# Kernel optimization log

Hardware: AMD Instinct MI355X
Metric: run time of the kernel (lower is better)

## Reference

```python
import jax, jax.numpy as jnp
import numpy as np

NUM_HEADS = 16


def setup_inputs() -> dict:
    key = jax.random.key(0)
    ks = jax.random.split(key, 5)
    b, s, d = 2, 2048, 1024
    std = (2.0 / (d + d)) ** 0.5
    x = jax.random.normal(ks[0], (b, s, d), dtype=jnp.float32)
    Wq = jax.random.normal(ks[1], (d, d), dtype=jnp.float32) * std
    Wk = jax.random.normal(ks[2], (d, d), dtype=jnp.float32) * std
    Wv = jax.random.normal(ks[3], (d, d), dtype=jnp.float32) * std
    Wo = jax.random.normal(ks[4], (d, d), dtype=jnp.float32) * std
    return {"x": x, "Wq": Wq, "Wk": Wk, "Wv": Wv, "Wo": Wo}


def reference(x, Wq, Wk, Wv, Wo):
    b, s, d = x.shape
    h = NUM_HEADS
    dk = d // h
    # projections: bias-free x @ W (W is [in, out])
    def split_heads(t):
        return t.reshape(b, s, h, dk).transpose(0, 2, 1, 3)  # b h s dk
    q = split_heads(x @ Wq)
    k = split_heads(x @ Wk)
    v = split_heads(x @ Wv)
    scale = 1.0 / jnp.sqrt(jnp.asarray(dk, dtype=x.dtype))
    scores = jnp.einsum('bhqd,bhkd->bhqk', q, k) * scale  # b h s s
    causal = jnp.tril(jnp.ones((s, s), dtype=bool))
    scores = jnp.where(causal, scores, -jnp.inf)
    probs = jax.nn.softmax(scores, axis=-1)
    out = jnp.einsum('bhqk,bhkd->bhqd', probs, v)
    out = out.transpose(0, 2, 1, 3).reshape(b, s, d)  # b s (h dk)
    return out @ Wo
```

## Files before the change

### kernel.cpp

```cpp
#include <hip/hip_runtime.h>

typedef unsigned short u16;
typedef unsigned int   u32;

using bf16x8 = __attribute__((ext_vector_type(8))) __bf16;
using bf16x4 = __attribute__((ext_vector_type(4))) __bf16;
using f32x4  = __attribute__((ext_vector_type(4))) float;
using s16x4  = __attribute__((ext_vector_type(4))) short;

#define NH    16
#define DKH   64
#define SEQ   2048
#define BAT   2
#define DMOD  1024

#define QSCALE 0.18033688011112042f

__device__ __forceinline__ u16 f2bf(float f) {
  union { float f; u32 u; } v; v.f = f;
  u32 r = v.u + 0x7fffu + ((v.u >> 16) & 1u);
  return (u16)(r >> 16);
}

__device__ __forceinline__ u32 pack2bf(float a, float b) {
  union { float f; u32 u; } x, y; x.f = a; y.f = b;
  u32 ua = x.u + 0x7fffu + ((x.u >> 16) & 1u);
  u32 ub = y.u + 0x7fffu + ((y.u >> 16) & 1u);
  return __builtin_amdgcn_perm(ub, ua, 0x07060302u);
}

__device__ __forceinline__ s16x4 pk4bf(float a, float b, float c, float d) {
  union { bf16x4 bv; s16x4 sv; } u;
  u.bv[0] = (__bf16)a; u.bv[1] = (__bf16)b; u.bv[2] = (__bf16)c; u.bv[3] = (__bf16)d;
  return u.sv;
}

#if __has_builtin(__builtin_amdgcn_exp2f)
#define EXP2(x) __builtin_amdgcn_exp2f(x)
#else
#define EXP2(x) exp2f(x)
#endif

#if __has_builtin(__builtin_amdgcn_mfma_f32_16x16x16bf16_1k)
__device__ __forceinline__ f32x4 mfma16(s16x4 a, s16x4 b, f32x4 c) {
  return __builtin_amdgcn_mfma_f32_16x16x16bf16_1k(a, b, c, 0, 0, 0);
}
#else
__device__ __forceinline__ f32x4 mfma16(s16x4 a, s16x4 b, f32x4 c) {
  f32x4 d;
  asm volatile("v_mfma_f32_16x16x16_bf16 %0, %1, %2, %3\n\ts_nop 7\n\ts_nop 7"
               : "=v"(d) : "v"(a), "v"(b), "v"(c));
  return d;
}
#endif

typedef const __attribute__((address_space(1))) u32 glb_u32;
typedef __attribute__((address_space(3))) u32 lds_u32;
__device__ __forceinline__ void gload16(const u16* g, u16* l) {
  __builtin_amdgcn_global_load_lds((glb_u32*)(const void*)g, (lds_u32*)(void*)l, 16, 0, 0);
}

__global__ __launch_bounds__(256) void transpose_all(const float* __restrict__ Wq,
                                                     const float* __restrict__ Wk,
                                                     const float* __restrict__ Wv,
                                                     const float* __restrict__ Wo,
                                                     u16* __restrict__ Wt) {
  __shared__ u16 t[32][33];
  const float* W = blockIdx.z == 0 ? Wq : blockIdx.z == 1 ? Wk : blockIdx.z == 2 ? Wv : Wo;
  u16* o = Wt + (size_t)blockIdx.z * DMOD * DMOD;
  int bx = blockIdx.x * 32, by = blockIdx.y * 32;
  int x = threadIdx.x, y = threadIdx.y;
  #pragma unroll
  for (int i = 0; i < 32; i += 8)
    t[y + i][x] = f2bf(W[(size_t)(by + y + i) * DMOD + bx + x]);
  __syncthreads();
  #pragma unroll
  for (int i = 0; i < 32; i += 8)
    o[(size_t)(bx + y + i) * DMOD + by + x] = t[x][y + i];
}

__global__ __launch_bounds__(256) void convert_x(const float* __restrict__ x,
                                                 u16* __restrict__ xb) {
  size_t i = ((size_t)blockIdx.x * 256 + threadIdx.x) * 8;
  float4 f0 = *(const float4*)(x + i);
  float4 f1 = *(const float4*)(x + i + 4);
  uint4 o;
  o.x = pack2bf(f0.x, f0.y); o.y = pack2bf(f0.z, f0.w);
  o.z = pack2bf(f1.x, f1.y); o.w = pack2bf(f1.z, f1.w);
  *(uint4*)(xb + i) = o;
}

__global__ __launch_bounds__(256, 3) void gemm_qkv(const u16* __restrict__ A,
                                                   const u16* __restrict__ Bt,
                                                   u16* __restrict__ Qo,
                                                   u16* __restrict__ Ko,
                                                   u16* __restrict__ Vo) {
  __shared__ __align__(16) u16 As[128 * 32];
  __shared__ __align__(16) u16 Bs[128 * 32];
  const int tid  = threadIdx.x;
  const int lane = tid & 63, wv = tid >> 6;
  const int wm   = wv >> 1, wn = wv & 1;
  const int lrow = lane & 15, quad = lane >> 4;
  const int tileM = blockIdx.x * 128, tileN = blockIdx.y * 128;

  const f32x4 fz = {0.f, 0.f, 0.f, 0.f};
  f32x4 acc[4][4];
  #pragma unroll
  for (int i = 0; i < 4; ++i)
    #pragma unroll
    for (int j = 0; j < 4; ++j) acc[i][j] = fz;

  for (int kt = 0; kt < DMOD; kt += 32) {
    if (kt) __syncthreads();
    #pragma unroll
    for (int i = 0; i < 2; ++i) {
      int idx = i * 256 + tid;
      gload16(&A [(size_t)(tileM + (idx >> 2)) * DMOD + kt + (idx & 3) * 8], &As[idx * 8]);
      gload16(&Bt[(size_t)(tileN + (idx >> 2)) * DMOD + kt + (idx & 3) * 8], &Bs[idx * 8]);
    }
    __syncthreads();

    bf16x8 af[4], bfr[4];
    #pragma unroll
    for (int mt = 0; mt < 4; ++mt)
      af[mt] = *(const bf16x8*)(&As[(wm * 64 + mt * 16 + lrow) * 32 + quad * 8]);
    #pragma unroll
    for (int nt = 0; nt < 4; ++nt)
      bfr[nt] = *(const bf16x8*)(&Bs[(wn * 64 + nt * 16 + lrow) * 32 + quad * 8]);
    #pragma unroll
    for (int mt = 0; mt < 4; ++mt)
      #pragma unroll
      for (int nt = 0; nt < 4; ++nt)
        acc[mt][nt] = __builtin_amdgcn_mfma_f32_16x16x32_bf16(af[mt], bfr[nt],
                                                              acc[mt][nt], 0, 0, 0);
  }

  #pragma unroll
  for (int mt = 0; mt < 4; ++mt) {
    #pragma unroll
    for (int nt = 0; nt < 4; ++nt) {
      int gm0 = tileM + wm * 64 + mt * 16 + quad * 4;
      int gn  = tileN + wn * 64 + nt * 16 + lrow;
      int which = gn >> 10, col = gn & 1023;
      int bb = gm0 >> 11, srw0 = gm0 & (SEQ - 1);
      int hh = col >> 6, dki = col & (DKH - 1);
      size_t bhi = (size_t)(bb * NH + hh);
      if (which == 0) {
        #pragma unroll
        for (int r = 0; r < 4; ++r)
          Qo[(bhi * SEQ + srw0 + r) * DKH + dki] = f2bf(acc[mt][nt][r] * QSCALE);
      } else if (which == 1) {
        #pragma unroll
        for (int r = 0; r < 4; ++r)
          Ko[(bhi * SEQ + srw0 + r) * DKH + dki] = f2bf(acc[mt][nt][r]);
      } else {
        uint2 pk;
        pk.x = pack2bf(acc[mt][nt][0], acc[mt][nt][1]);
        pk.y = pack2bf(acc[mt][nt][2], acc[mt][nt][3]);
        *(uint2*)(&Vo[(((bhi * (SEQ / 4)) + (srw0 >> 2)) * DKH + dki) * 4]) = pk;
      }
    }
  }
}

__global__ __launch_bounds__(256, 3) void gemm_out(const u16* __restrict__ A,
                                                   const u16* __restrict__ Bt,
                                                   float* __restrict__ Co) {
  __shared__ __align__(16) u16 As[128 * 32];
  __shared__ __align__(16) u16 Bs[64 * 32];
  const int tid  = threadIdx.x;
  const int lane = tid & 63, wv = tid >> 6;
  const int wm   = wv & 1, wn = wv >> 1;
  const int lrow = lane & 15, quad = lane >> 4;
  const int tileM = blockIdx.x * 128, tileN = blockIdx.y * 64;

  const f32x4 fz = {0.f, 0.f, 0.f, 0.f};
  f32x4 acc[4][2];
  #pragma unroll
  for (int i = 0; i < 4; ++i) { acc[i][0] = fz; acc[i][1] = fz; }

  for (int kt = 0; kt < DMOD; kt += 32) {
    if (kt) __syncthreads();
    #pragma unroll
    for (int i = 0; i < 2; ++i) {
      int idx = i * 256 + tid;
      gload16(&A[(size_t)(tileM + (idx >> 2)) * DMOD + kt + (idx & 3) * 8], &As[idx * 8]);
    }
    gload16(&Bt[(size_t)(tileN + (tid >> 2)) * DMOD + kt + (tid & 3) * 8], &Bs[tid * 8]);
    __syncthreads();

    bf16x8 af[4], bfr[2];
    #pragma unroll
    for (int mt = 0; mt < 4; ++mt)
      af[mt] = *(const bf16x8*)(&As[(wm * 64 + mt * 16 + lrow) * 32 + quad * 8]);
    #pragma unroll
    for (int nt = 0; nt < 2; ++nt)
      bfr[nt] = *(const bf16x8*)(&Bs[(wn * 32 + nt * 16 + lrow) * 32 + quad * 8]);
    #pragma unroll
    for (int mt = 0; mt < 4; ++mt)
      #pragma unroll
      for (int nt = 0; nt < 2; ++nt)
        acc[mt][nt] = __builtin_amdgcn_mfma_f32_16x16x32_bf16(af[mt], bfr[nt],
                                                              acc[mt][nt], 0, 0, 0);
  }

  #pragma unroll
  for (int mt = 0; mt < 4; ++mt)
    #pragma unroll
    for (int nt = 0; nt < 2; ++nt)
      #pragma unroll
      for (int r = 0; r < 4; ++r) {
        int gm = tileM + wm * 64 + mt * 16 + quad * 4 + r;
        int gn = tileN + wn * 32 + nt * 16 + lrow;
        Co[(size_t)gm * DMOD + gn] = acc[mt][nt][r];
      }
}

#define OP 68

__global__ __launch_bounds__(128, 2) void attn_k(const u16* __restrict__ Q,
                                                 const u16* __restrict__ Kg,
                                                 const u16* __restrict__ Vg,
                                                 u16* __restrict__ Og) {
  __shared__ __align__(16) u16 Ks[128 * 64];
  __shared__ __align__(16) u16 Vs[32 * 256];

  const int tid  = threadIdx.x;
  const int lane = tid & 63, w = tid >> 6;
  const int lrow = lane & 15, quad = lane >> 4;
  const int bh = blockIdx.x;
  const int qb = (int)((blockIdx.y + bh) & 31);
  const int b = bh >> 4, h = bh & 15;
  const int jmax = qb >> 1;
  const int qoff = qb & 1;

  const u16* Qbh = Q  + (size_t)bh * SEQ * DKH;
  const u16* Kbh = Kg + (size_t)bh * SEQ * DKH;
  const u16* Vbh = Vg + (size_t)bh * SEQ * DKH;

  bf16x8 bq[2][2];
  #pragma unroll
  for (int s = 0; s < 2; ++s)
    #pragma unroll
    for (int kk = 0; kk < 2; ++kk)
      bq[s][kk] = *(const bf16x8*)(&Qbh[(size_t)(qb * 64 + (2 * w + s) * 16 + lrow) * DKH
                                        + kk * 32 + quad * 8]);

  const f32x4 fz = {0.f, 0.f, 0.f, 0.f};
  f32x4 oacc[2][4];
  #pragma unroll
  for (int s = 0; s < 2; ++s)
    #pragma unroll
    for (int d = 0; d < 4; ++d) oacc[s][d] = fz;
  float lsum[2] = {0.f, 0.f};

  for (int j = 0; j <= jmax; ++j) {
    if (j) __syncthreads();

    #pragma unroll
    for (int i = 0; i < 8; ++i) {
      int cD = i * 128 + tid;
      int r = cD >> 3, c = cD & 7;
      gload16(&Kbh[(size_t)(j * 128 + r) * DKH + ((c ^ (r & 7)) << 3)], &Ks[cD * 8]);
    }
    #pragma unroll
    for (int i = 0; i < 8; ++i) {
      int cD = i * 128 + tid;
      int sq = cD >> 5, c = cD & 31;
      gload16(&Vbh[(size_t)(j * 32 + sq) * 256 + ((c ^ (sq & 7)) << 3)], &Vs[cD * 8]);
    }

    __syncthreads();

    if (j < jmax) {
      __builtin_amdgcn_s_setprio(1);
      f32x4 sacc[2][8];
      #pragma unroll
      for (int s = 0; s < 2; ++s)
        #pragma unroll
        for (int m = 0; m < 8; ++m) sacc[s][m] = fz;
      #pragma unroll
      for (int kk = 0; kk < 2; ++kk)
        #pragma unroll
        for (int m = 0; m < 8; ++m) {
          bf16x8 ak = *(const bf16x8*)(&Ks[(m * 16 + lrow) * 64
                                           + (((kk * 4 + quad) ^ (lrow & 7)) << 3)]);
          sacc[0][m] = __builtin_amdgcn_mfma_f32_16x16x32_bf16(ak, bq[0][kk], sacc[0][m], 0, 0, 0);
          sacc[1][m] = __builtin_amdgcn_mfma_f32_16x16x32_bf16(ak, bq[1][kk], sacc[1][m], 0, 0, 0);
        }
      #pragma unroll
      for (int m = 0; m < 8; ++m) {
        float p00 = EXP2(sacc[0][m][0]), p01 = EXP2(sacc[0][m][1]);
        float p02 = EXP2(sacc[0][m][2]), p03 = EXP2(sacc[0][m][3]);
        float p10 = EXP2(sacc[1][m][0]), p11 = EXP2(sacc[1][m][1]);
        float p12 = EXP2(sacc[1][m][2]), p13 = EXP2(sacc[1][m][3]);
        lsum[0] += (p00 + p01) + (p02 + p03);
        lsum[1] += (p10 + p11) + (p12 + p13);
        s16x4 pk0 = pk4bf(p00, p01, p02, p03);
        s16x4 pk1 = pk4bf(p10, p11, p12, p13);
        const int sq = m * 4 + quad;
        #pragma unroll
        for (int d = 0; d < 4; ++d) {
          int dk = d * 16 + lrow;
          s16x4 av = *(const s16x4*)(&Vs[sq * 256
                                         + ((((dk >> 1) ^ (sq & 7)) << 3) | ((dk & 1) << 2))]);
          oacc[0][d] = mfma16(av, pk0, oacc[0][d]);
          oacc[1][d] = mfma16(av, pk1, oacc[1][d]);
        }
      }
      __builtin_amdgcn_s_setprio(0);
    } else {
      #pragma unroll
      for (int s = 0; s < 2; ++s) {
        const int L = qoff * 4 + 2 * w + s;
        for (int m = 0; m < L; ++m) {
          f32x4 sv = fz;
          #pragma unroll
          for (int kk = 0; kk < 2; ++kk) {
            bf16x8 ak = *(const bf16x8*)(&Ks[(m * 16 + lrow) * 64
                                             + (((kk * 4 + quad) ^ (lrow & 7)) << 3)]);
            sv = __builtin_amdgcn_mfma_f32_16x16x32_bf16(ak, bq[s][kk], sv, 0, 0, 0);
          }
          float p0 = EXP2(sv[0]), p1 = EXP2(sv[1]), p2 = EXP2(sv[2]), p3 = EXP2(sv[3]);
          lsum[s] += (p0 + p1) + (p2 + p3);
          s16x4 pk = pk4bf(p0, p1, p2, p3);
          const int sq = m * 4 + quad;
          #pragma unroll
          for (int d = 0; d < 4; ++d) {
            int dk = d * 16 + lrow;
            s16x4 av = *(const s16x4*)(&Vs[sq * 256
                                           + ((((dk >> 1) ^ (sq & 7)) << 3) | ((dk & 1) << 2))]);
            oacc[s][d] = mfma16(av, pk, oacc[s][d]);
          }
        }
        {
          f32x4 sv = fz;
          #pragma unroll
          for (int kk = 0; kk < 2; ++kk) {
            bf16x8 ak = *(const bf16x8*)(&Ks[(L * 16 + lrow) * 64
                                             + (((kk * 4 + quad) ^ (lrow & 7)) << 3)]);
            sv = __builtin_amdgcn_mfma_f32_16x16x32_bf16(ak, bq[s][kk], sv, 0, 0, 0);
          }
          float p[4];
          #pragma unroll
          for (int r = 0; r < 4; ++r)
            p[r] = (quad * 4 + r > lrow) ? 0.f : EXP2(sv[r]);
          lsum[s] += (p[0] + p[1]) + (p[2] + p[3]);
          s16x4 pk = pk4bf(p[0], p[1], p[2], p[3]);
          const int sq = L * 4 + quad;
          #pragma unroll
          for (int d = 0; d < 4; ++d) {
            int dk = d * 16 + lrow;
            s16x4 av = *(const s16x4*)(&Vs[sq * 256
                                           + ((((dk >> 1) ^ (sq & 7)) << 3) | ((dk & 1) << 2))]);
            oacc[s][d] = mfma16(av, pk, oacc[s][d]);
          }
        }
      }
    }
  }

  float inv[2];
  #pragma unroll
  for (int s = 0; s < 2; ++s) {
    float v = lsum[s];
    v += __shfl_xor(v, 16, 64);
    v += __shfl_xor(v, 32, 64);
    inv[s] = 1.f / v;
  }

  __syncthreads();
  u16* Osr = Ks;
  #pragma unroll
  for (int s = 0; s < 2; ++s) {
    int row = (2 * w + s) * 16 + lrow;
    #pragma unroll
    for (int d = 0; d < 4; ++d) {
      uint2 pkk;
      pkk.x = pack2bf(oacc[s][d][0] * inv[s], oacc[s][d][1] * inv[s]);
      pkk.y = pack2bf(oacc[s][d][2] * inv[s], oacc[s][d][3] * inv[s]);
      *(uint2*)(&Osr[row * OP + d * 16 + quad * 4]) = pkk;
    }
  }
  __syncthreads();
  #pragma unroll
  for (int k = 0; k < 4; ++k) {
    int c = k * 128 + tid;
    int row = c >> 3, ch = c & 7;
    uint4 v = *(const uint4*)(&Osr[row * OP + ch * 8]);
    *(uint4*)(&Og[(size_t)(b * SEQ + qb * 64 + row) * DMOD + h * DKH + ch * 8]) = v;
  }
}

extern "C" void kernel_launch(void* const* d_in, const int* in_sizes, int n_in,
                              void* d_out, int out_size, void* d_ws, size_t ws_size,
                              hipStream_t stream) {
  const float* x  = (const float*)d_in[0];
  const float* Wq = (const float*)d_in[1];
  const float* Wk = (const float*)d_in[2];
  const float* Wv = (const float*)d_in[3];
  const float* Wo = (const float*)d_in[4];

  u16* ws = (u16*)d_ws;
  const size_t WSZ = (size_t)DMOD * DMOD;
  const size_t TSZ = (size_t)BAT * NH * SEQ * DKH;
  u16* Wt  = ws;
  u16* Wto = Wt + 3 * WSZ;
  u16* xb  = Wt + 4 * WSZ;
  u16* Qb  = xb + TSZ;
  u16* Kb  = Qb + TSZ;
  u16* Vb  = Kb + TSZ;
  u16* Ob  = xb;

  transpose_all<<<dim3(32, 32, 4), dim3(32, 8), 0, stream>>>(Wq, Wk, Wv, Wo, Wt);
  convert_x<<<dim3(2048), 256, 0, stream>>>(x, xb);

  gemm_qkv<<<dim3(32, 24), 256, 0, stream>>>(xb, Wt, Qb, Kb, Vb);

  attn_k<<<dim3(32, 32), 128, 0, stream>>>(Qb, Kb, Vb, Ob);

  gemm_out<<<dim3(32, 16), 256, 0, stream>>>(Ob, Wto, (float*)d_out);
}
```

Measured before the change: 178.4 us.

## Pair causal query blocks per workgroup and double-buffer K/V tiles

Each attention workgroup now handles two query blocks, y and 31-y, so every block runs the same 17 K/V tile iterations and the causal triangle is balanced. The grid is halved to match. K/V tiles are double-buffered in LDS, with the next tile's global-to-LDS copy issued before computing on the current tile, to overlap memory loads with MFMA work. This roughly doubles LDS usage, which may lower occupancy, and adds a mid-loop output flush plus a Q reload.

```diff
diff --git a/kernel.cpp b/kernel.cpp
--- a/kernel.cpp
+++ b/kernel.cpp
@@ -222,17 +222,20 @@
                                                  const u16* __restrict__ Kg,
                                                  const u16* __restrict__ Vg,
                                                  u16* __restrict__ Og) {
-  __shared__ __align__(16) u16 Ks[128 * 64];
-  __shared__ __align__(16) u16 Vs[32 * 256];
+  __shared__ __align__(16) u16 KsA[128 * 64];
+  __shared__ __align__(16) u16 VsA[32 * 256];
+  __shared__ __align__(16) u16 KsB[128 * 64];
+  __shared__ __align__(16) u16 VsB[32 * 256];
+  __shared__ __align__(16) u16 Os[64 * OP];
 
   const int tid  = threadIdx.x;
   const int lane = tid & 63, w = tid >> 6;
   const int lrow = lane & 15, quad = lane >> 4;
   const int bh = blockIdx.x;
-  const int qb = (int)((blockIdx.y + bh) & 31);
+  const int y  = blockIdx.y;
   const int b = bh >> 4, h = bh & 15;
-  const int jmax = qb >> 1;
-  const int qoff = qb & 1;
+  const int qA = y, qB = 31 - y;
+  const int tA = y >> 1;
 
   const u16* Qbh = Q  + (size_t)bh * SEQ * DKH;
   const u16* Kbh = Kg + (size_t)bh * SEQ * DKH;
@@ -243,8 +246,29 @@
   for (int s = 0; s < 2; ++s)
     #pragma unroll
     for (int kk = 0; kk < 2; ++kk)
-      bq[s][kk] = *(const bf16x8*)(&Qbh[(size_t)(qb * 64 + (2 * w + s) * 16 + lrow) * DKH
+      bq[s][kk] = *(const bf16x8*)(&Qbh[(size_t)(qA * 64 + (2 * w + s) * 16 + lrow) * DKH
                                         + kk * 32 + quad * 8]);
+
+#define STAGE(Kd, Vd, jn)                                                              \
+  {                                                                                    \
+    _Pragma("unroll")                                                                  \
+    for (int i_ = 0; i_ < 8; ++i_) {                                                   \
+      int cD = i_ * 128 + tid;                                                         \
+      int r_ = cD >> 3, c_ = cD & 7;                                                   \
+      gload16(&Kbh[(size_t)((jn) * 128 + r_) * DKH + ((c_ ^ (r_ & 7)) << 3)],          \
+              &(Kd)[cD * 8]);                                                          \
+    }                                                                                  \
+    _Pragma("unroll")                                                                  \
+    for (int i_ = 0; i_ < 8; ++i_) {                                                   \
+      int cD = i_ * 128 + tid;                                                         \
+      int sq_ = cD >> 5, c_ = cD & 31;                                                 \
+      gload16(&Vbh[(size_t)((jn) * 32 + sq_) * 256 + ((c_ ^ (sq_ & 7)) << 3)],         \
+              &(Vd)[cD * 8]);                                                          \
+    }                                                                                  \
+  }
+
+  STAGE(KsA, VsA, 0);
+  __syncthreads();
 
   const f32x4 fz = {0.f, 0.f, 0.f, 0.f};
   f32x4 oacc[2][4];
@@ -254,25 +278,23 @@
     for (int d = 0; d < 4; ++d) oacc[s][d] = fz;
   float lsum[2] = {0.f, 0.f};
 
-  for (int j = 0; j <= jmax; ++j) {
-    if (j) __syncthreads();
-
-    #pragma unroll
-    for (int i = 0; i < 8; ++i) {
-      int cD = i * 128 + tid;
-      int r = cD >> 3, c = cD & 7;
-      gload16(&Kbh[(size_t)(j * 128 + r) * DKH + ((c ^ (r & 7)) << 3)], &Ks[cD * 8]);
+  int cur = 0;
+  for (int t = 0; t < 17; ++t) {
+    const int half = (t > tA) ? 1 : 0;
+    const int qcur = half ? qB : qA;
+    u16* Ks = cur ? KsB : KsA;
+    u16* Vs = cur ? VsB : VsA;
+    u16* Kn = cur ? KsA : KsB;
+    u16* Vn = cur ? VsA : VsB;
+
+    if (t < 16) {
+      const int tn = t + 1;
+      const int jn = (tn > tA) ? (tn - tA - 1) : tn;
+      STAGE(Kn, Vn, jn);
     }
-    #pragma unroll
-    for (int i = 0; i < 8; ++i) {
-      int cD = i * 128 + tid;
-      int sq = cD >> 5, c = cD & 31;
-      gload16(&Vbh[(size_t)(j * 32 + sq) * 256 + ((c ^ (sq & 7)) << 3)], &Vs[cD * 8]);
-    }
-
-    __syncthreads();
-
-    if (j < jmax) {
+
+    const bool diag = (t == tA) || (t == 16);
+    if (!diag) {
       __builtin_amdgcn_s_setprio(1);
       f32x4 sacc[2][8];
       #pragma unroll
@@ -310,6 +332,7 @@
       }
       __builtin_amdgcn_s_setprio(0);
     } else {
+      const int qoff = qcur & 1;
       #pragma unroll
       for (int s = 0; s < 2; ++s) {
         const int L = qoff * 4 + 2 * w + s;
@@ -357,39 +380,54 @@
           }
         }
       }
+
+      float inv[2];
+      #pragma unroll
+      for (int s = 0; s < 2; ++s) {
+        float v = lsum[s];
+        v += __shfl_xor(v, 16, 64);
+        v += __shfl_xor(v, 32, 64);
+        inv[s] = 1.f / v;
+      }
+      #pragma unroll
+      for (int s = 0; s < 2; ++s) {
+        int row = (2 * w + s) * 16 + lrow;
+        #pragma unroll
+        for (int d = 0; d < 4; ++d) {
+          uint2 pkk;
+          pkk.x = pack2bf(oacc[s][d][0] * inv[s], oacc[s][d][1] * inv[s]);
+          pkk.y = pack2bf(oacc[s][d][2] * inv[s], oacc[s][d][3] * inv[s]);
+          *(uint2*)(&Os[row * OP + d * 16 + quad * 4]) = pkk;
+        }
+      }
+      __syncthreads();
+      #pragma unroll
+      for (int k = 0; k < 4; ++k) {
+        int c = k * 128 + tid;
+        int row = c >> 3, ch = c & 7;
+        uint4 v = *(const uint4*)(&Os[row * OP + ch * 8]);
+        *(uint4*)(&Og[(size_t)(b * SEQ + qcur * 64 + row) * DMOD + h * DKH + ch * 8]) = v;
+      }
+
+      if (!half) {
+        #pragma unroll
+        for (int s = 0; s < 2; ++s)
+          #pragma unroll
+          for (int d = 0; d < 4; ++d) oacc[s][d] = fz;
+        lsum[0] = 0.f; lsum[1] = 0.f;
+        #pragma unroll
+        for (int s = 0; s < 2; ++s)
+          #pragma unroll
+          for (int kk = 0; kk < 2; ++kk)
+            bq[s][kk] = *(const bf16x8*)(&Qbh[(size_t)(qB * 64 + (2 * w + s) * 16 + lrow) * DKH
+                                              + kk * 32 + quad * 8]);
+      }
     }
+
+    __syncthreads();
+    cur ^= 1;
   }
-
-  float inv[2];
-  #pragma unroll
-  for (int s = 0; s < 2; ++s) {
-    float v = lsum[s];
-    v += __shfl_xor(v, 16, 64);
-    v += __shfl_xor(v, 32, 64);
-    inv[s] = 1.f / v;
-  }
-
-  __syncthreads();
-  u16* Osr = Ks;
-  #pragma unroll
-  for (int s = 0; s < 2; ++s) {
-    int row = (2 * w + s) * 16 + lrow;
-    #pragma unroll
-    for (int d = 0; d < 4; ++d) {
-      uint2 pkk;
-      pkk.x = pack2bf(oacc[s][d][0] * inv[s], oacc[s][d][1] * inv[s]);
-      pkk.y = pack2bf(oacc[s][d][2] * inv[s], oacc[s][d][3] * inv[s]);
-      *(uint2*)(&Osr[row * OP + d * 16 + quad * 4]) = pkk;
-    }
-  }
-  __syncthreads();
-  #pragma unroll
-  for (int k = 0; k < 4; ++k) {
-    int c = k * 128 + tid;
-    int row = c >> 3, ch = c & 7;
-    uint4 v = *(const uint4*)(&Osr[row * OP + ch * 8]);
-    *(uint4*)(&Og[(size_t)(b * SEQ + qb * 64 + row) * DMOD + h * DKH + ch * 8]) = v;
-  }
+#undef STAGE
 }
 
 extern "C" void kernel_launch(void* const* d_in, const int* in_sizes, int n_in,
@@ -417,7 +455,7 @@
 
   gemm_qkv<<<dim3(32, 24), 256, 0, stream>>>(xb, Wt, Qb, Kb, Vb);
 
-  attn_k<<<dim3(32, 32), 128, 0, stream>>>(Qb, Kb, Vb, Ob);
+  attn_k<<<dim3(32, 16), 128, 0, stream>>>(Qb, Kb, Vb, Ob);
 
   gemm_out<<<dim3(32, 16), 256, 0, stream>>>(Ob, Wto, (float*)d_out);
 }
```

Result: faster. 174.2 us (-2.4%).

## Pair causal query tiles per block with split-K warp groups and double-buffered KV

Applied to the files above, without the earlier changes.

The attention kernel now gives each 256-thread block two complementary 64-row query tiles (y and 31-y), which balances causal work across blocks and halves the grid. Two warp groups each take alternating 64-key chunks and merge partial outputs and row sums through shared memory at the end. K/V tiles are double-buffered so the next chunk's loads are issued before the current one is computed. This adds LDS use and extra reductions and barriers, which may limit occupancy.

```diff
diff --git a/kernel.cpp b/kernel.cpp
--- a/kernel.cpp
+++ b/kernel.cpp
@@ -216,180 +216,245 @@
       }
 }
 
-#define OP 68
-
-__global__ __launch_bounds__(128, 2) void attn_k(const u16* __restrict__ Q,
+#define OPAD 68
+
+__global__ __launch_bounds__(256, 2) void attn_k(const u16* __restrict__ Q,
                                                  const u16* __restrict__ Kg,
                                                  const u16* __restrict__ Vg,
                                                  u16* __restrict__ Og) {
-  __shared__ __align__(16) u16 Ks[128 * 64];
-  __shared__ __align__(16) u16 Vs[32 * 256];
+  __shared__ __align__(16) u16 Ksb[2][2][64 * 64];
+  __shared__ __align__(16) u16 Vsb[2][2][16 * 256];
+  __shared__ __align__(16) u16 Osc[64 * OPAD];
+  __shared__ float Lsc[32];
 
   const int tid  = threadIdx.x;
   const int lane = tid & 63, w = tid >> 6;
+  const int g    = w >> 1,  wg = w & 1;
   const int lrow = lane & 15, quad = lane >> 4;
-  const int bh = blockIdx.x;
-  const int qb = (int)((blockIdx.y + bh) & 31);
+  const int bh = blockIdx.x, y = blockIdx.y;
   const int b = bh >> 4, h = bh & 15;
-  const int jmax = qb >> 1;
-  const int qoff = qb & 1;
+  const int qB = 31 - y;
+  const int sAend = y >> 1;
 
   const u16* Qbh = Q  + (size_t)bh * SEQ * DKH;
   const u16* Kbh = Kg + (size_t)bh * SEQ * DKH;
   const u16* Vbh = Vg + (size_t)bh * SEQ * DKH;
 
-  bf16x8 bq[2][2];
-  #pragma unroll
-  for (int s = 0; s < 2; ++s)
-    #pragma unroll
-    for (int kk = 0; kk < 2; ++kk)
-      bq[s][kk] = *(const bf16x8*)(&Qbh[(size_t)(qb * 64 + (2 * w + s) * 16 + lrow) * DKH
-                                        + kk * 32 + quad * 8]);
-
   const f32x4 fz = {0.f, 0.f, 0.f, 0.f};
   f32x4 oacc[2][4];
-  #pragma unroll
-  for (int s = 0; s < 2; ++s)
-    #pragma unroll
-    for (int d = 0; d < 4; ++d) oacc[s][d] = fz;
-  float lsum[2] = {0.f, 0.f};
-
-  for (int j = 0; j <= jmax; ++j) {
-    if (j) __syncthreads();
-
-    #pragma unroll
-    for (int i = 0; i < 8; ++i) {
-      int cD = i * 128 + tid;
-      int r = cD >> 3, c = cD & 7;
-      gload16(&Kbh[(size_t)(j * 128 + r) * DKH + ((c ^ (r & 7)) << 3)], &Ks[cD * 8]);
-    }
-    #pragma unroll
-    for (int i = 0; i < 8; ++i) {
-      int cD = i * 128 + tid;
-      int sq = cD >> 5, c = cD & 31;
-      gload16(&Vbh[(size_t)(j * 32 + sq) * 256 + ((c ^ (sq & 7)) << 3)], &Vs[cD * 8]);
-    }
-
+  float lsum[2];
+  bf16x8 bq[2][2];
+
+#define DEC(s_, g_, qt_, j_, v_)                                                   \
+  { if ((s_) <= sAend) { qt_ = y;  j_ = 2 * (s_) + (g_);              v_ = (j_ <= y);  } \
+    else               { qt_ = qB; j_ = 2 * ((s_) - sAend - 1) + (g_); v_ = (j_ <= qB); } }
+
+#define STAGE1(gg, p_, j_)                                                          \
+  { _Pragma("unroll")                                                               \
+    for (int i_ = 0; i_ < 2; ++i_) {                                                \
+      int cD = i_ * 256 + tid; int r_ = cD >> 3, c_ = cD & 7;                       \
+      gload16(&Kbh[(size_t)((j_) * 64 + r_) * DKH + ((c_ ^ (r_ & 7)) << 3)],        \
+              &Ksb[gg][p_][cD * 8]); }                                              \
+    _Pragma("unroll")                                                               \
+    for (int i_ = 0; i_ < 2; ++i_) {                                                \
+      int cD = i_ * 256 + tid; int sq_ = cD >> 5, c_ = cD & 31;                     \
+      gload16(&Vbh[(size_t)((j_) * 16 + sq_) * 256 + ((c_ ^ (sq_ & 7)) << 3)],      \
+              &Vsb[gg][p_][cD * 8]); } }
+
+#define LOADQ(qt_)                                                                  \
+  { _Pragma("unroll")                                                               \
+    for (int s_ = 0; s_ < 2; ++s_)                                                  \
+      _Pragma("unroll")                                                             \
+      for (int kk_ = 0; kk_ < 2; ++kk_)                                             \
+        bq[s_][kk_] = *(const bf16x8*)(&Qbh[(size_t)((qt_) * 64 + wg * 32 + s_ * 16 \
+                                            + lrow) * DKH + kk_ * 32 + quad * 8]); }
+
+  auto EPI = [&](int qt) {
+    float ls[2];
+    #pragma unroll
+    for (int s2 = 0; s2 < 2; ++s2) {
+      float v = lsum[s2];
+      v += __shfl_xor(v, 16, 64);
+      v += __shfl_xor(v, 32, 64);
+      ls[s2] = v;
+    }
+    float* OscF = (float*)Osc;
+    #pragma unroll
+    for (int ph = 0; ph < 2; ++ph) {
+      if (g == 1) {
+        int srow = wg * 16 + lrow;
+        #pragma unroll
+        for (int d = 0; d < 4; ++d)
+          *(f32x4*)(&OscF[srow * OPAD + d * 16 + quad * 4]) = oacc[ph][d];
+        if (quad == 0) Lsc[srow] = ls[ph];
+      }
+      __syncthreads();
+      if (g == 0) {
+        int srow = wg * 16 + lrow;
+        ls[ph] += Lsc[srow];
+        #pragma unroll
+        for (int d = 0; d < 4; ++d) {
+          f32x4 ov = *(const f32x4*)(&OscF[srow * OPAD + d * 16 + quad * 4]);
+          oacc[ph][d] += ov;
+        }
+      }
+      __syncthreads();
+    }
+    if (g == 0) {
+      #pragma unroll
+      for (int s2 = 0; s2 < 2; ++s2) {
+        float inv = 1.f / ls[s2];
+        int row = wg * 32 + s2 * 16 + lrow;
+        #pragma unroll
+        for (int d = 0; d < 4; ++d) {
+          uint2 pkk;
+          pkk.x = pack2bf(oacc[s2][d][0] * inv, oacc[s2][d][1] * inv);
+          pkk.y = pack2bf(oacc[s2][d][2] * inv, oacc[s2][d][3] * inv);
+          *(uint2*)(&Osc[row * OPAD + d * 16 + quad * 4]) = pkk;
+        }
+      }
+    }
     __syncthreads();
-
-    if (j < jmax) {
-      __builtin_amdgcn_s_setprio(1);
-      f32x4 sacc[2][8];
-      #pragma unroll
-      for (int s = 0; s < 2; ++s)
-        #pragma unroll
-        for (int m = 0; m < 8; ++m) sacc[s][m] = fz;
-      #pragma unroll
-      for (int kk = 0; kk < 2; ++kk)
-        #pragma unroll
-        for (int m = 0; m < 8; ++m) {
-          bf16x8 ak = *(const bf16x8*)(&Ks[(m * 16 + lrow) * 64
-                                           + (((kk * 4 + quad) ^ (lrow & 7)) << 3)]);
-          sacc[0][m] = __builtin_amdgcn_mfma_f32_16x16x32_bf16(ak, bq[0][kk], sacc[0][m], 0, 0, 0);
-          sacc[1][m] = __builtin_amdgcn_mfma_f32_16x16x32_bf16(ak, bq[1][kk], sacc[1][m], 0, 0, 0);
-        }
-      #pragma unroll
-      for (int m = 0; m < 8; ++m) {
-        float p00 = EXP2(sacc[0][m][0]), p01 = EXP2(sacc[0][m][1]);
-        float p02 = EXP2(sacc[0][m][2]), p03 = EXP2(sacc[0][m][3]);
-        float p10 = EXP2(sacc[1][m][0]), p11 = EXP2(sacc[1][m][1]);
-        float p12 = EXP2(sacc[1][m][2]), p13 = EXP2(sacc[1][m][3]);
-        lsum[0] += (p00 + p01) + (p02 + p03);
-        lsum[1] += (p10 + p11) + (p12 + p13);
-        s16x4 pk0 = pk4bf(p00, p01, p02, p03);
-        s16x4 pk1 = pk4bf(p10, p11, p12, p13);
-        const int sq = m * 4 + quad;
-        #pragma unroll
-        for (int d = 0; d < 4; ++d) {
-          int dk = d * 16 + lrow;
-          s16x4 av = *(const s16x4*)(&Vs[sq * 256
-                                         + ((((dk >> 1) ^ (sq & 7)) << 3) | ((dk & 1) << 2))]);
-          oacc[0][d] = mfma16(av, pk0, oacc[0][d]);
-          oacc[1][d] = mfma16(av, pk1, oacc[1][d]);
-        }
-      }
-      __builtin_amdgcn_s_setprio(0);
-    } else {
-      #pragma unroll
-      for (int s = 0; s < 2; ++s) {
-        const int L = qoff * 4 + 2 * w + s;
-        for (int m = 0; m < L; ++m) {
-          f32x4 sv = fz;
+    #pragma unroll
+    for (int k2 = 0; k2 < 2; ++k2) {
+      int c2 = k2 * 256 + tid;
+      int row = c2 >> 3, ch = c2 & 7;
+      uint4 vv = *(const uint4*)(&Osc[row * OPAD + ch * 8]);
+      *(uint4*)(&Og[(size_t)(b * SEQ + qt * 64 + row) * DMOD + h * DKH + ch * 8]) = vv;
+    }
+  };
+
+  { int qt0, j0; bool v0;
+    DEC(0, 0, qt0, j0, v0); if (v0) STAGE1(0, 0, j0);
+    DEC(0, 1, qt0, j0, v0); if (v0) STAGE1(1, 0, j0);
+  }
+  LOADQ(y);
+  #pragma unroll
+  for (int s2 = 0; s2 < 2; ++s2) {
+    oacc[s2][0] = fz; oacc[s2][1] = fz; oacc[s2][2] = fz; oacc[s2][3] = fz;
+    lsum[s2] = 0.f;
+  }
+  __syncthreads();
+
+  for (int s = 0; s <= 16; ++s) {
+    const int p = s & 1;
+
+    if (s < 16) {
+      int qtn, jn; bool vn;
+      DEC(s + 1, 0, qtn, jn, vn); if (vn) STAGE1(0, p ^ 1, jn);
+      DEC(s + 1, 1, qtn, jn, vn); if (vn) STAGE1(1, p ^ 1, jn);
+    }
+
+    int qt, j; bool valid;
+    DEC(s, g, qt, j, valid);
+    if (valid) {
+      const u16* Ks = Ksb[g][p];
+      const u16* Vs = Vsb[g][p];
+      if (j < qt) {
+        __builtin_amdgcn_s_setprio(1);
+        f32x4 sacc[2][4];
+        #pragma unroll
+        for (int s2 = 0; s2 < 2; ++s2)
           #pragma unroll
-          for (int kk = 0; kk < 2; ++kk) {
+          for (int m = 0; m < 4; ++m) sacc[s2][m] = fz;
+        #pragma unroll
+        for (int kk = 0; kk < 2; ++kk)
+          #pragma unroll
+          for (int m = 0; m < 4; ++m) {
             bf16x8 ak = *(const bf16x8*)(&Ks[(m * 16 + lrow) * 64
                                              + (((kk * 4 + quad) ^ (lrow & 7)) << 3)]);
-            sv = __builtin_amdgcn_mfma_f32_16x16x32_bf16(ak, bq[s][kk], sv, 0, 0, 0);
+            sacc[0][m] = __builtin_amdgcn_mfma_f32_16x16x32_bf16(ak, bq[0][kk], sacc[0][m], 0, 0, 0);
+            sacc[1][m] = __builtin_amdgcn_mfma_f32_16x16x32_bf16(ak, bq[1][kk], sacc[1][m], 0, 0, 0);
           }
-          float p0 = EXP2(sv[0]), p1 = EXP2(sv[1]), p2 = EXP2(sv[2]), p3 = EXP2(sv[3]);
-          lsum[s] += (p0 + p1) + (p2 + p3);
-          s16x4 pk = pk4bf(p0, p1, p2, p3);
+        #pragma unroll
+        for (int m = 0; m < 4; ++m) {
+          float p00 = EXP2(sacc[0][m][0]), p01 = EXP2(sacc[0][m][1]);
+          float p02 = EXP2(sacc[0][m][2]), p03 = EXP2(sacc[0][m][3]);
+          float p10 = EXP2(sacc[1][m][0]), p11 = EXP2(sacc[1][m][1]);
+          float p12 = EXP2(sacc[1][m][2]), p13 = EXP2(sacc[1][m][3]);
+          lsum[0] += (p00 + p01) + (p02 + p03);
+          lsum[1] += (p10 + p11) + (p12 + p13);
+          s16x4 pk0 = pk4bf(p00, p01, p02, p03);
+          s16x4 pk1 = pk4bf(p10, p11, p12, p13);
           const int sq = m * 4 + quad;
           #pragma unroll
           for (int d = 0; d < 4; ++d) {
             int dk = d * 16 + lrow;
             s16x4 av = *(const s16x4*)(&Vs[sq * 256
                                            + ((((dk >> 1) ^ (sq & 7)) << 3) | ((dk & 1) << 2))]);
-            oacc[s][d] = mfma16(av, pk, oacc[s][d]);
+            oacc[0][d] = mfma16(av, pk0, oacc[0][d]);
+            oacc[1][d] = mfma16(av, pk1, oacc[1][d]);
           }
         }
-        {
-          f32x4 sv = fz;
-          #pragma unroll
-          for (int kk = 0; kk < 2; ++kk) {
-            bf16x8 ak = *(const bf16x8*)(&Ks[(L * 16 + lrow) * 64
-                                             + (((kk * 4 + quad) ^ (lrow & 7)) << 3)]);
-            sv = __builtin_amdgcn_mfma_f32_16x16x32_bf16(ak, bq[s][kk], sv, 0, 0, 0);
+        __builtin_amdgcn_s_setprio(0);
+      } else {
+        #pragma unroll
+        for (int s2 = 0; s2 < 2; ++s2) {
+          const int L = 2 * wg + s2;
+          for (int m = 0; m < L; ++m) {
+            f32x4 sv = fz;
+            #pragma unroll
+            for (int kk = 0; kk < 2; ++kk) {
+              bf16x8 ak = *(const bf16x8*)(&Ks[(m * 16 + lrow) * 64
+                                               + (((kk * 4 + quad) ^ (lrow & 7)) << 3)]);
+              sv = __builtin_amdgcn_mfma_f32_16x16x32_bf16(ak, bq[s2][kk], sv, 0, 0, 0);
+            }
+            float p0 = EXP2(sv[0]), p1 = EXP2(sv[1]), p2 = EXP2(sv[2]), p3 = EXP2(sv[3]);
+            lsum[s2] += (p0 + p1) + (p2 + p3);
+            s16x4 pk = pk4bf(p0, p1, p2, p3);
+            const int sq = m * 4 + quad;
+            #pragma unroll
+            for (int d = 0; d < 4; ++d) {
+              int dk = d * 16 + lrow;
+              s16x4 av = *(const s16x4*)(&Vs[sq * 256
+                                             + ((((dk >> 1) ^ (sq & 7)) << 3) | ((dk & 1) << 2))]);
+              oacc[s2][d] = mfma16(av, pk, oacc[s2][d]);
+            }
           }
-          float p[4];
-          #pragma unroll
-          for (int r = 0; r < 4; ++r)
-            p[r] = (quad * 4 + r > lrow) ? 0.f : EXP2(sv[r]);
-          lsum[s] += (p[0] + p[1]) + (p[2] + p[3]);
-          s16x4 pk = pk4bf(p[0], p[1], p[2], p[3]);
-          const int sq = L * 4 + quad;
-          #pragma unroll
-          for (int d = 0; d < 4; ++d) {
-            int dk = d * 16 + lrow;
-            s16x4 av = *(const s16x4*)(&Vs[sq * 256
-                                           + ((((dk >> 1) ^ (sq & 7)) << 3) | ((dk & 1) << 2))]);
-            oacc[s][d] = mfma16(av, pk, oacc[s][d]);
+          {
+            f32x4 sv = fz;
+            #pragma unroll
+            for (int kk = 0; kk < 2; ++kk) {
+              bf16x8 ak = *(const bf16x8*)(&Ks[(L * 16 + lrow) * 64
+                                               + (((kk * 4 + quad) ^ (lrow & 7)) << 3)]);
+              sv = __builtin_amdgcn_mfma_f32_16x16x32_bf16(ak, bq[s2][kk], sv, 0, 0, 0);
+            }
+            float pp[4];
+            #pragma unroll
+            for (int r = 0; r < 4; ++r)
+              pp[r] = (quad * 4 + r > lrow) ? 0.f : EXP2(sv[r]);
+            lsum[s2] += (pp[0] + pp[1]) + (pp[2] + pp[3]);
+            s16x4 pk = pk4bf(pp[0], pp[1], pp[2], pp[3]);
+            const int sq = L * 4 + quad;
+            #pragma unroll
+            for (int d = 0; d < 4; ++d) {
+              int dk = d * 16 + lrow;
+              s16x4 av = *(const s16x4*)(&Vs[sq * 256
+                                             + ((((dk >> 1) ^ (sq & 7)) << 3) | ((dk & 1) << 2))]);
+              oacc[s2][d] = mfma16(av, pk, oacc[s2][d]);
+            }
           }
         }
       }
     }
-  }
-
-  float inv[2];
-  #pragma unroll
-  for (int s = 0; s < 2; ++s) {
-    float v = lsum[s];
-    v += __shfl_xor(v, 16, 64);
-    v += __shfl_xor(v, 32, 64);
-    inv[s] = 1.f / v;
-  }
-
-  __syncthreads();
-  u16* Osr = Ks;
-  #pragma unroll
-  for (int s = 0; s < 2; ++s) {
-    int row = (2 * w + s) * 16 + lrow;
-    #pragma unroll
-    for (int d = 0; d < 4; ++d) {
-      uint2 pkk;
-      pkk.x = pack2bf(oacc[s][d][0] * inv[s], oacc[s][d][1] * inv[s]);
-      pkk.y = pack2bf(oacc[s][d][2] * inv[s], oacc[s][d][3] * inv[s]);
-      *(uint2*)(&Osr[row * OP + d * 16 + quad * 4]) = pkk;
-    }
-  }
-  __syncthreads();
-  #pragma unroll
-  for (int k = 0; k < 4; ++k) {
-    int c = k * 128 + tid;
-    int row = c >> 3, ch = c & 7;
-    uint4 v = *(const uint4*)(&Osr[row * OP + ch * 8]);
-    *(uint4*)(&Og[(size_t)(b * SEQ + qb * 64 + row) * DMOD + h * DKH + ch * 8]) = v;
-  }
+
+    __syncthreads();
+
+    if (s == sAend) {
+      EPI(y);
+      #pragma unroll
+      for (int s2 = 0; s2 < 2; ++s2) {
+        oacc[s2][0] = fz; oacc[s2][1] = fz; oacc[s2][2] = fz; oacc[s2][3] = fz;
+        lsum[s2] = 0.f;
+      }
+      LOADQ(qB);
+    } else if (s == 16) {
+      EPI(qB);
+    }
+  }
+#undef DEC
+#undef STAGE1
+#undef LOADQ
 }
 
 extern "C" void kernel_launch(void* const* d_in, const int* in_sizes, int n_in,
@@ -417,7 +482,7 @@
 
   gemm_qkv<<<dim3(32, 24), 256, 0, stream>>>(xb, Wt, Qb, Kb, Vb);
 
-  attn_k<<<dim3(32, 32), 128, 0, stream>>>(Qb, Kb, Vb, Ob);
+  attn_k<<<dim3(32, 16), 256, 0, stream>>>(Qb, Kb, Vb, Ob);
 
   gemm_out<<<dim3(32, 16), 256, 0, stream>>>(Ob, Wto, (float*)d_out);
 }
```

Result: faster. 170.4 us (-4.5%).
